# Kernel tuning notes

Hardware: AMD Instinct MI355X
Metric: run time of the kernel (lower is better)

The kernel has to match this reference:

```python
import jax, jax.numpy as jnp
import numpy as np

NUM_CAPSULE = 16
DIM_CAPSULE = 16
NUM_ROUTING = 3
EPS = 1e-7  # K.epsilon()


def squash(v, axis=-1):
    s2 = jnp.sum(jnp.square(v), axis=axis, keepdims=True) + EPS
    scale = s2 / ((1.0 + s2) * jnp.sqrt(s2))
    return scale * v


def setup_inputs() -> dict:
    key = jax.random.key(0)
    k1, k2 = jax.random.split(key)
    B, N, IC, ID = 64, 128, 32, 8
    x = jax.random.normal(k1, (B, N, IC, ID), dtype=jnp.float32)
    # glorot_uniform for W: [IC, ID, NUM_CAPSULE*DIM_CAPSULE]
    fan_in, fan_out = ID, NUM_CAPSULE * DIM_CAPSULE
    limit = np.sqrt(6.0 / (fan_in + fan_out))
    W = jax.random.uniform(k2, (IC, ID, NUM_CAPSULE * DIM_CAPSULE), dtype=jnp.float32,
                           minval=-limit, maxval=limit)
    return {"x": x, "W": W}


def reference(x, W):
    B, N, IC, ID = x.shape
    NC, DC = NUM_CAPSULE, DIM_CAPSULE
    u = x.reshape(-1, IC, ID)  # [BN, IC, ID]
    # prediction vectors: [BN, IC, NC*DC] -> [BN, NC, IC, DC]
    u_hat = jnp.einsum('bij,ijk->bik', u, W).reshape(-1, IC, NC, DC).transpose(0, 2, 1, 3)
    u_hat_stopped = jax.lax.stop_gradient(u_hat)
    b = jnp.zeros((u_hat.shape[0], NC, IC), dtype=x.dtype)
    outputs = None
    for i in range(NUM_ROUTING):
        c = jax.nn.softmax(b, axis=1)  # softmax over num_capsule axis (dim=1 in source)
        hat = u_hat if i == NUM_ROUTING - 1 else u_hat_stopped
        outputs = squash(jnp.einsum('bci,bcid->bcd', c, hat))  # [BN, NC, DC]
        if i < NUM_ROUTING - 1:
            b = b + jnp.einsum('bcd,bcid->bci', outputs, u_hat_stopped)
    return outputs.reshape(B, N, NC, DC)
```

## Files before the change

kernel.cpp:

```cpp
#include <hip/hip_runtime.h>
#include <hip/hip_bf16.h>


#define S 2

typedef float    v2f __attribute__((ext_vector_type(2)));
typedef _Float16 v2h __attribute__((ext_vector_type(2)));

template <int CTRL>
__device__ __forceinline__ float dppf(float x) {
  return __builtin_bit_cast(float,
      __builtin_amdgcn_update_dpp(0, __builtin_bit_cast(int, x), CTRL, 0xF, 0xF, true));
}
template <int CTRL>
__device__ __forceinline__ v2f dpp2(v2f v) {
  v2f r;
  r.x = dppf<CTRL>(v.x);
  r.y = dppf<CTRL>(v.y);
  return r;
}
template <int CTRL, int BANK>
__device__ __forceinline__ float dpp_old(float old, float x) {
  return __builtin_bit_cast(float,
      __builtin_amdgcn_update_dpp(__builtin_bit_cast(int, old),
                                  __builtin_bit_cast(int, x), CTRL, 0xF, BANK, false));
}
__device__ __forceinline__ float xor4t(float s) {
  float ya = dpp_old<0x104, 0x5>(0.0f, s);
  return dpp_old<0x114, 0xA>(ya, s);
}

#if __has_builtin(__builtin_amdgcn_fdot2)
__device__ __forceinline__ float dot2(v2h a, v2h b, float c) {
  return __builtin_amdgcn_fdot2(a, b, c, false);
}
#else
__device__ __forceinline__ float dot2(v2h a, v2h b, float c) {
  return fmaf((float)a.x, (float)b.x, fmaf((float)a.y, (float)b.y, c));
}
#endif

__global__ __launch_bounds__(256) void prep_kernel(const float* __restrict__ W,
                                                   const float* __restrict__ x,
                                                   _Float16* __restrict__ Wth,
                                                   _Float16* __restrict__ xh) {
  int bid = blockIdx.x;
  if (bid < 256) {
    int o       = bid * 256 + threadIdx.x;
    int ic_slot = o >> 11;
    int k       = (o >> 3) & 255;
    int id      = o & 7;
    int ic_src  = (ic_slot & 16) | ((ic_slot ^ k) & 15);
    Wth[o] = (_Float16)W[(ic_src * 8 + id) * 256 + k];
  } else {
    int tid = (bid - 256) * 256 + threadIdx.x;
    const float4* xp = (const float4*)x + tid * 2;
    float4 f0 = xp[0], f1 = xp[1];
    v2h h0 = {(_Float16)f0.x, (_Float16)f0.y};
    v2h h1 = {(_Float16)f0.z, (_Float16)f0.w};
    v2h h2 = {(_Float16)f1.x, (_Float16)f1.y};
    v2h h3 = {(_Float16)f1.z, (_Float16)f1.w};
    uint4 o;
    o.x = __builtin_bit_cast(unsigned, h0);
    o.y = __builtin_bit_cast(unsigned, h1);
    o.z = __builtin_bit_cast(unsigned, h2);
    o.w = __builtin_bit_cast(unsigned, h3);
    ((uint4*)xh)[tid] = o;
  }
}

__device__ __forceinline__ v2f squash2(v2f o) {
  v2f s2 = o * o;
  s2.x += dppf<0xB1>(s2.x);   s2.y += dppf<0xB1>(s2.y);
  s2.x += dppf<0x4E>(s2.x);   s2.y += dppf<0x4E>(s2.y);
  s2.x += dppf<0x141>(s2.x);  s2.y += dppf<0x141>(s2.y);
  s2.x += dppf<0x140>(s2.x);  s2.y += dppf<0x140>(s2.y);
  s2 += (v2f){1e-7f, 1e-7f};
  v2f sc;
  sc.x = s2.x * __builtin_amdgcn_rsqf(s2.x) * __builtin_amdgcn_rcpf(1.f + s2.x);
  sc.y = s2.y * __builtin_amdgcn_rsqf(s2.y) * __builtin_amdgcn_rcpf(1.f + s2.y);
  return o * sc;
}

template <bool ASSIGN>
__device__ __forceinline__ void b_update2(v2f v, const v2f* uhx, int dc,
                                          float* bp0, float* bp1) {
#pragma unroll
  for (int icb = 0; icb < 32; icb += 16) {
    v2f y[16];
#pragma unroll
    for (int j = 0; j < 16; ++j) y[j] = v * uhx[icb + j];
#pragma unroll
    for (int j = 0; j < 8; ++j) {
      y[j].x += dppf<0x128>(y[j + 8].x);
      y[j].y += dppf<0x128>(y[j + 8].y);
    }
#pragma unroll
    for (int j = 0; j < 4; ++j) {
      y[j].x += xor4t(y[j + 4].x);
      y[j].y += xor4t(y[j + 4].y);
    }
#pragma unroll
    for (int j = 0; j < 2; ++j) {
      y[j].x += dppf<0x4E>(y[j + 2].x);
      y[j].y += dppf<0x4E>(y[j + 2].y);
    }
    y[0].x += dppf<0xB1>(y[1].x);
    y[0].y += dppf<0xB1>(y[1].y);
    if (ASSIGN) { bp0[icb + dc] = y[0].x;  bp1[icb + dc] = y[0].y; }
    else        { bp0[icb + dc] += y[0].x; bp1[icb + dc] += y[0].y; }
  }
}

__global__ __launch_bounds__(256, 3) void caps_kernel(const unsigned* __restrict__ xh32,
                                                      const uint4* __restrict__ Wt4,
                                                      float* __restrict__ out) {
  const int t  = threadIdx.x;
  const int nc = t >> 4;
  const int dc = t & 15;
  const int s0 = blockIdx.x * S;

  __shared__ float b_lds[S][16][33];
  __shared__ float c_lds[16][66];
  __shared__ __align__(16) _Float16 xh_lds[2 * 256];

  ((unsigned*)xh_lds)[t] = xh32[s0 * 128 + t];
  __syncthreads();

  v2f uhx[32];
  v2f o2 = (v2f){0.f, 0.f};

#pragma unroll
  for (int ic = 0; ic < 32; ++ic) {
    uint4 wv = Wt4[ic * 256 + t];
    v2h w0 = __builtin_bit_cast(v2h, wv.x);
    v2h w1 = __builtin_bit_cast(v2h, wv.y);
    v2h w2 = __builtin_bit_cast(v2h, wv.z);
    v2h w3 = __builtin_bit_cast(v2h, wv.w);
    const int icx0 = (ic & 16) | ((ic ^ dc) & 15);
    uint4 xv0 = *(const uint4*)(xh_lds + icx0 * 8);
    uint4 xv1 = *(const uint4*)(xh_lds + 256 + icx0 * 8);
    float a0 = dot2(__builtin_bit_cast(v2h, xv0.w), w3,
               dot2(__builtin_bit_cast(v2h, xv0.z), w2,
               dot2(__builtin_bit_cast(v2h, xv0.y), w1,
               dot2(__builtin_bit_cast(v2h, xv0.x), w0, 0.f))));
    float a1 = dot2(__builtin_bit_cast(v2h, xv1.w), w3,
               dot2(__builtin_bit_cast(v2h, xv1.z), w2,
               dot2(__builtin_bit_cast(v2h, xv1.y), w1,
               dot2(__builtin_bit_cast(v2h, xv1.x), w0, 0.f))));
    v2f u = (v2f){a0, a1};
    uhx[ic] = u;
    o2 += u;
  }

  {
    v2f v = squash2(o2 * (v2f){0.0625f, 0.0625f});
    b_update2<true>(v, uhx, dc, &b_lds[0][nc][0], &b_lds[1][nc][0]);
  }
  __syncthreads();

#pragma unroll
  for (int r = 1; r < 3; ++r) {
    {
      const int ss  = t >> 7;
      const int icc = (t >> 2) & 31;
      const int q   = t & 3;
      float e0 = __expf(b_lds[ss][4 * q + 0][icc]);
      float e1 = __expf(b_lds[ss][4 * q + 1][icc]);
      float e2 = __expf(b_lds[ss][4 * q + 2][icc]);
      float e3 = __expf(b_lds[ss][4 * q + 3][icc]);
      float ps = (e0 + e1) + (e2 + e3);
      ps += dppf<0xB1>(ps);
      ps += dppf<0x4E>(ps);
      float inv = __builtin_amdgcn_rcpf(ps);
      c_lds[4 * q + 0][2 * icc + ss] = e0 * inv;
      c_lds[4 * q + 1][2 * icc + ss] = e1 * inv;
      c_lds[4 * q + 2][2 * icc + ss] = e2 * inv;
      c_lds[4 * q + 3][2 * icc + ss] = e3 * inv;
    }
    __syncthreads();

    const float2* cpair = (const float2*)&c_lds[nc][0];
    v2f o = (v2f){0.f, 0.f};
#pragma unroll
    for (int j = 0; j < 16; ++j) {
      const int m = j ^ dc;
      float2 cA = cpair[m];
      float2 cB = cpair[m + 16];
      o = __builtin_elementwise_fma((v2f){cA.x, cA.y}, uhx[j], o);
      o = __builtin_elementwise_fma((v2f){cB.x, cB.y}, uhx[16 + j], o);
    }
    v2f v = squash2(o);
    if (r == 2) {
      out[(s0 + 0) * 256 + t] = v.x;
      out[(s0 + 1) * 256 + t] = v.y;
    } else {
      b_update2<false>(v, uhx, dc, &b_lds[0][nc][0], &b_lds[1][nc][0]);
      __syncthreads();
    }
  }
}

extern "C" void kernel_launch(void* const* d_in, const int* in_sizes, int n_in,
                              void* d_out, int out_size, void* d_ws, size_t ws_size,
                              hipStream_t stream) {
  const float* x = (const float*)d_in[0];
  const float* W = (const float*)d_in[1];
  _Float16* Wth = (_Float16*)d_ws;
  _Float16* xh  = (_Float16*)d_ws + 65536;

  prep_kernel<<<1280, 256, 0, stream>>>(W, x, Wth, xh);
  caps_kernel<<<8192 / S, 256, 0, stream>>>((const unsigned*)xh, (const uint4*)Wth,
                                            (float*)d_out);
}
```

Measured before the change: 97.25 us.

## Store prediction vectors and routing math in packed fp16, raise occupancy

Keeps the per-thread u_hat registers as packed half2 instead of float2, and runs the routing weighted sum, agreement dot products and DPP reductions in packed fp16 arithmetic. Routing coefficients are also stored as fp16 in LDS. Halving the register footprint allows launch bounds to request 4 blocks per SM instead of 3, and packed math halves the ALU and DPP instruction count. The cost is reduced accuracy, because fp16 accumulation over 32 terms and fp16 softmax coefficients may exceed the tolerance.

```diff
diff --git a/kernel.cpp b/kernel.cpp
--- a/kernel.cpp
+++ b/kernel.cpp
@@ -6,6 +6,10 @@
 
 typedef float    v2f __attribute__((ext_vector_type(2)));
 typedef _Float16 v2h __attribute__((ext_vector_type(2)));
+
+__device__ __forceinline__ v2h pack2h(float a, float b) {
+  return __builtin_bit_cast(v2h, __builtin_amdgcn_cvt_pkrtz(a, b));
+}
 
 template <int CTRL>
 __device__ __forceinline__ float dppf(float x) {
@@ -13,21 +17,18 @@
       __builtin_amdgcn_update_dpp(0, __builtin_bit_cast(int, x), CTRL, 0xF, 0xF, true));
 }
 template <int CTRL>
-__device__ __forceinline__ v2f dpp2(v2f v) {
-  v2f r;
-  r.x = dppf<CTRL>(v.x);
-  r.y = dppf<CTRL>(v.y);
-  return r;
+__device__ __forceinline__ v2h dpph(v2h v) {
+  return __builtin_bit_cast(v2h,
+      __builtin_amdgcn_update_dpp(0, __builtin_bit_cast(int, v), CTRL, 0xF, 0xF, true));
 }
 template <int CTRL, int BANK>
-__device__ __forceinline__ float dpp_old(float old, float x) {
-  return __builtin_bit_cast(float,
-      __builtin_amdgcn_update_dpp(__builtin_bit_cast(int, old),
-                                  __builtin_bit_cast(int, x), CTRL, 0xF, BANK, false));
-}
-__device__ __forceinline__ float xor4t(float s) {
-  float ya = dpp_old<0x104, 0x5>(0.0f, s);
-  return dpp_old<0x114, 0xA>(ya, s);
+__device__ __forceinline__ int dpp_old_i(int old, int x) {
+  return __builtin_amdgcn_update_dpp(old, x, CTRL, 0xF, BANK, false);
+}
+__device__ __forceinline__ v2h xor4t_h(v2h s) {
+  int si = __builtin_bit_cast(int, s);
+  int ya = dpp_old_i<0x104, 0x5>(0, si);
+  return __builtin_bit_cast(v2h, dpp_old_i<0x114, 0xA>(ya, si));
 }
 
 #if __has_builtin(__builtin_amdgcn_fdot2)
@@ -83,36 +84,27 @@
 }
 
 template <bool ASSIGN>
-__device__ __forceinline__ void b_update2(v2f v, const v2f* uhx, int dc,
+__device__ __forceinline__ void b_update2(v2h vh, const v2h* uhx, int dc,
                                           float* bp0, float* bp1) {
 #pragma unroll
   for (int icb = 0; icb < 32; icb += 16) {
-    v2f y[16];
-#pragma unroll
-    for (int j = 0; j < 16; ++j) y[j] = v * uhx[icb + j];
-#pragma unroll
-    for (int j = 0; j < 8; ++j) {
-      y[j].x += dppf<0x128>(y[j + 8].x);
-      y[j].y += dppf<0x128>(y[j + 8].y);
-    }
-#pragma unroll
-    for (int j = 0; j < 4; ++j) {
-      y[j].x += xor4t(y[j + 4].x);
-      y[j].y += xor4t(y[j + 4].y);
-    }
-#pragma unroll
-    for (int j = 0; j < 2; ++j) {
-      y[j].x += dppf<0x4E>(y[j + 2].x);
-      y[j].y += dppf<0x4E>(y[j + 2].y);
-    }
-    y[0].x += dppf<0xB1>(y[1].x);
-    y[0].y += dppf<0xB1>(y[1].y);
-    if (ASSIGN) { bp0[icb + dc] = y[0].x;  bp1[icb + dc] = y[0].y; }
-    else        { bp0[icb + dc] += y[0].x; bp1[icb + dc] += y[0].y; }
-  }
-}
-
-__global__ __launch_bounds__(256, 3) void caps_kernel(const unsigned* __restrict__ xh32,
+    v2h y[16];
+#pragma unroll
+    for (int j = 0; j < 16; ++j) y[j] = vh * uhx[icb + j];
+#pragma unroll
+    for (int j = 0; j < 8; ++j) y[j] += dpph<0x128>(y[j + 8]);
+#pragma unroll
+    for (int j = 0; j < 4; ++j) y[j] += xor4t_h(y[j + 4]);
+#pragma unroll
+    for (int j = 0; j < 2; ++j) y[j] += dpph<0x4E>(y[j + 2]);
+    y[0] += dpph<0xB1>(y[1]);
+    float e0 = (float)y[0].x, e1 = (float)y[0].y;
+    if (ASSIGN) { bp0[icb + dc] = e0;  bp1[icb + dc] = e1; }
+    else        { bp0[icb + dc] += e0; bp1[icb + dc] += e1; }
+  }
+}
+
+__global__ __launch_bounds__(256, 4) void caps_kernel(const unsigned* __restrict__ xh32,
                                                       const uint4* __restrict__ Wt4,
                                                       float* __restrict__ out) {
   const int t  = threadIdx.x;
@@ -121,13 +113,13 @@
   const int s0 = blockIdx.x * S;
 
   __shared__ float b_lds[S][16][33];
-  __shared__ float c_lds[16][66];
+  __shared__ _Float16 c16h[16][32][2];
   __shared__ __align__(16) _Float16 xh_lds[2 * 256];
 
   ((unsigned*)xh_lds)[t] = xh32[s0 * 128 + t];
   __syncthreads();
 
-  v2f uhx[32];
+  v2h uhx[32];
   v2f o2 = (v2f){0.f, 0.f};
 
 #pragma unroll
@@ -148,14 +140,14 @@
                dot2(__builtin_bit_cast(v2h, xv1.z), w2,
                dot2(__builtin_bit_cast(v2h, xv1.y), w1,
                dot2(__builtin_bit_cast(v2h, xv1.x), w0, 0.f))));
-    v2f u = (v2f){a0, a1};
-    uhx[ic] = u;
-    o2 += u;
+    o2 += (v2f){a0, a1};
+    uhx[ic] = pack2h(a0, a1);
   }
 
   {
     v2f v = squash2(o2 * (v2f){0.0625f, 0.0625f});
-    b_update2<true>(v, uhx, dc, &b_lds[0][nc][0], &b_lds[1][nc][0]);
+    v2h vh = pack2h(v.x, v.y);
+    b_update2<true>(vh, uhx, dc, &b_lds[0][nc][0], &b_lds[1][nc][0]);
   }
   __syncthreads();
 
@@ -173,29 +165,31 @@
       ps += dppf<0xB1>(ps);
       ps += dppf<0x4E>(ps);
       float inv = __builtin_amdgcn_rcpf(ps);
-      c_lds[4 * q + 0][2 * icc + ss] = e0 * inv;
-      c_lds[4 * q + 1][2 * icc + ss] = e1 * inv;
-      c_lds[4 * q + 2][2 * icc + ss] = e2 * inv;
-      c_lds[4 * q + 3][2 * icc + ss] = e3 * inv;
+      c16h[4 * q + 0][icc][ss] = (_Float16)(e0 * inv);
+      c16h[4 * q + 1][icc][ss] = (_Float16)(e1 * inv);
+      c16h[4 * q + 2][icc][ss] = (_Float16)(e2 * inv);
+      c16h[4 * q + 3][icc][ss] = (_Float16)(e3 * inv);
     }
     __syncthreads();
 
-    const float2* cpair = (const float2*)&c_lds[nc][0];
-    v2f o = (v2f){0.f, 0.f};
+    const v2h* crow = (const v2h*)&c16h[nc][0][0];
+    v2h oh = (v2h){(_Float16)0.f, (_Float16)0.f};
 #pragma unroll
     for (int j = 0; j < 16; ++j) {
       const int m = j ^ dc;
-      float2 cA = cpair[m];
-      float2 cB = cpair[m + 16];
-      o = __builtin_elementwise_fma((v2f){cA.x, cA.y}, uhx[j], o);
-      o = __builtin_elementwise_fma((v2f){cB.x, cB.y}, uhx[16 + j], o);
+      v2h cA = crow[m];
+      v2h cB = crow[m + 16];
+      oh = __builtin_elementwise_fma(cA, uhx[j], oh);
+      oh = __builtin_elementwise_fma(cB, uhx[16 + j], oh);
     }
+    v2f o = (v2f){(float)oh.x, (float)oh.y};
     v2f v = squash2(o);
     if (r == 2) {
       out[(s0 + 0) * 256 + t] = v.x;
       out[(s0 + 1) * 256 + t] = v.y;
     } else {
-      b_update2<false>(v, uhx, dc, &b_lds[0][nc][0], &b_lds[1][nc][0]);
+      v2h vh = pack2h(v.x, v.y);
+      b_update2<false>(vh, uhx, dc, &b_lds[0][nc][0], &b_lds[1][nc][0]);
       __syncthreads();
     }
   }
```

Result: no change. 98.51 us (+1.3%).
